# Kernel tuning notes

Measured on AMD Instinct MI355X. Metric: run time of the kernel, lower is better.

## Reference

```python
import jax
jax.config.update("jax_enable_x64", True)
import jax.numpy as jnp
import numpy as np

CKA_WEIGHT = 0.1


def _group_cka_sum(feats):
    """feats: [F, N, D] float. Returns sum of pairwise CKA over all (i,j) pairs.

    Faithful to CKASR: K = X X^T with zeroed diagonal, unbiased HSIC
    (Song et al. estimator), CKA[i,j] = HSIC(Ki,Kj)/sqrt(HSIC(Ki,Ki)HSIC(Kj,Kj)).
    All pairwise loops are batched into einsums.
    """
    F, N, D = feats.shape
    X = feats.reshape(F, N, D).astype(jnp.float64)
    K = jnp.einsum('fnd,fmd->fnm', X, X)                 # [F,N,N] Gram
    K = K * (1.0 - jnp.eye(N, dtype=K.dtype))            # fill_diagonal_(0)
    # HSIC(Ki, Kj) = 1/(N(N-3)) * ( tr(Ki Kj)
    #   + sum(Ki) sum(Kj) / ((N-1)(N-2))
    #   - 2/(N-2) * <rowsum(Ki), rowsum(Kj)> )
    trKL = jnp.einsum('iab,jab->ij', K, K)               # tr(Ki Kj), K symmetric
    s = jnp.sum(K, axis=(1, 2))                          # [F] total sums
    r = jnp.sum(K, axis=2)                               # [F,N] row sums
    rr = jnp.einsum('ia,ja->ij', r, r)                   # [F,F]
    hsic = (trKL + jnp.outer(s, s) / ((N - 1) * (N - 2))
            - 2.0 * rr / (N - 2)) / (N * (N - 3))        # [F,F]
    d = jnp.sqrt(jnp.diagonal(hsic))                     # [F]
    cka = hsic / (d[:, None] * d[None, :])
    return jnp.sum(cka)


def setup_inputs() -> dict:
    key = jax.random.key(0)
    k1, k2, k3, k4 = jax.random.split(key, 4)
    N, C = 64, 1000
    output = jax.random.normal(k1, (N, C), dtype=jnp.float32)
    target = jax.random.randint(k2, (N,), 0, C, dtype=jnp.int64)
    feats_a = jax.random.normal(k3, (3, N, 65536), dtype=jnp.float32)
    feats_b = jax.random.normal(k4, (4, N, 32768), dtype=jnp.float32)
    return {"output": output, "target": target,
            "feats_a": feats_a, "feats_b": feats_b}


def reference(output, target, feats_a, feats_b):
    N = output.shape[0]
    logp = jax.nn.log_softmax(output.astype(jnp.float32), axis=-1)
    ce = -jnp.mean(logp[jnp.arange(N), target])           # CrossEntropyLoss (mean)
    cka = _group_cka_sum(feats_a) + _group_cka_sum(feats_b)
    loss = ce + CKA_WEIGHT * cka.astype(jnp.float32)
    return (loss, output)
```

## Files before the change

### kernel.cpp

```cpp
#include <hip/hip_runtime.h>
#include <hip/hip_bf16.h>
#include <math.h>

typedef __attribute__((ext_vector_type(8))) short short8;
typedef __attribute__((ext_vector_type(4))) float f32x4;

#define PSTRIDE 4160
#define SLAB_A_F 8388608u
#define SLAB_B_F 4194304u

__device__ __forceinline__ unsigned int bf16_rn(float x) {
    unsigned int u = __float_as_uint(x);
    return (u + 0x7FFFu + ((u >> 16) & 1u)) >> 16;
}

__global__ __launch_bounds__(256) void ce_kernel(
    const float* __restrict__ logits, const int* __restrict__ target,
    float* __restrict__ out_copy, float* __restrict__ ce_rows)
{
    const int row = blockIdx.x;
    const float* x = logits + row * 1000;
    const int t = threadIdx.x;
    __shared__ float red[256];

    float m = -INFINITY;
    for (int i = t; i < 1000; i += 256) {
        float v = x[i];
        out_copy[row * 1000 + i] = v;
        m = fmaxf(m, v);
    }
    red[t] = m; __syncthreads();
    for (int s = 128; s > 0; s >>= 1) {
        if (t < s) red[t] = fmaxf(red[t], red[t + s]);
        __syncthreads();
    }
    m = red[0];
    __syncthreads();

    float ssum = 0.f;
    for (int i = t; i < 1000; i += 256) ssum += expf(x[i] - m);
    red[t] = ssum; __syncthreads();
    for (int s = 128; s > 0; s >>= 1) {
        if (t < s) red[t] += red[t + s];
        __syncthreads();
    }
    if (t == 0) {
        double lse = (double)m + log((double)red[0]);
        int tg = target[row];
        ce_rows[row] = (float)(-((double)x[tg] - lse));
    }
}

__global__ __launch_bounds__(256) void repack_kernel(
    const float* __restrict__ A, const float* __restrict__ B,
    char* __restrict__ slab, int nfA, int nfB)
{
    const int uA = nfA * 512;
    const int uTot = uA + nfB * 256;
    const int t = threadIdx.x;

    for (int u = blockIdx.x; u < uTot; u += gridDim.x) {
        const float* xr;
        char* slabF;
        int row, seg, D;
        if (u < uA) {
            int f = u >> 9, rem = u & 511;
            seg = rem & 7; row = rem >> 3; D = 65536;
            xr = A + ((size_t)(f * 64 + row)) * D;
            slabF = slab + (size_t)f * SLAB_A_F;
        } else {
            int v = u - uA;
            int f = v >> 8, rem = v & 255;
            seg = rem & 3; row = rem >> 2; D = 32768;
            xr = B + ((size_t)(f * 64 + row)) * D;
            slabF = slab + (size_t)nfA * SLAB_A_F + (size_t)f * SLAB_B_F;
        }
        const int k0 = seg * 8192;
        float4 va[4], vb[4];
#pragma unroll
        for (int i = 0; i < 4; ++i) {
            const float* p = xr + k0 + i * 2048 + t * 8;
            va[i] = *(const float4*)p;
            vb[i] = *(const float4*)(p + 4);
        }
#pragma unroll
        for (int i = 0; i < 4; ++i) {
            float vv[8] = {va[i].x, va[i].y, va[i].z, va[i].w,
                           vb[i].x, vb[i].y, vb[i].z, vb[i].w};
            short8 hv;
#pragma unroll
            for (int j = 0; j < 8; ++j) hv[j] = (short)bf16_rn(vv[j]);
            int kg = k0 + i * 2048 + t * 8;
            int chunk = kg >> 9, kk = kg & 511;
            *(short8*)(slabF + (size_t)chunk * 65536 + row * 1024 + kk * 2) = hv;
        }
    }
}

__global__ __launch_bounds__(256) void gram_kernel(
    const char* __restrict__ slab, float* __restrict__ partials,
    int nfA, int nfB)
{
    __shared__ float kbuf[4096];
    const int blk = blockIdx.x;
    const int f = blk >> 6, local = blk & 63;

    const char* slabF;
    int c0, nchunk;
    if (f < nfA) {
        slabF = slab + (size_t)f * SLAB_A_F;
        c0 = local * 2; nchunk = 2;
    } else {
        slabF = slab + (size_t)nfA * SLAB_A_F + (size_t)(f - nfA) * SLAB_B_F;
        c0 = local; nchunk = 1;
    }

    const int t = threadIdx.x;
    const int wave = t >> 6, lane = t & 63;
    const int m = lane & 15, quad = lane >> 4;
    const int loff = wave * 256 + quad * 16;

    f32x4 acc[4][4];
#pragma unroll
    for (int i = 0; i < 4; ++i)
#pragma unroll
        for (int j = 0; j < 4; ++j) acc[i][j] = (f32x4)0.f;

    for (int ci = 0; ci < nchunk; ++ci) {
        const char* cb = slabF + (size_t)(c0 + ci) * 65536;
        short8 fr[4][4];
#pragma unroll
        for (int s = 0; s < 4; ++s)
#pragma unroll
            for (int tm = 0; tm < 4; ++tm)
                fr[s][tm] = *(const short8*)(cb + (tm * 16 + m) * 1024
                                             + loff + s * 64);
#pragma unroll
        for (int s = 0; s < 4; ++s)
#pragma unroll
            for (int tm = 0; tm < 4; ++tm)
#pragma unroll
                for (int tn = 0; tn < 4; ++tn)
                    acc[tm][tn] = __builtin_amdgcn_mfma_f32_16x16x32_bf16(
                        fr[s][tm], fr[s][tn], acc[tm][tn], 0, 0, 0);
    }

    __syncthreads();
    if (wave == 0) {
#pragma unroll
        for (int tm = 0; tm < 4; ++tm)
#pragma unroll
            for (int tn = 0; tn < 4; ++tn)
#pragma unroll
                for (int r = 0; r < 4; ++r)
                    kbuf[(tm * 16 + quad * 4 + r) * 64 + tn * 16 + m] = acc[tm][tn][r];
    }
    __syncthreads();
    if (wave != 0) {
#pragma unroll
        for (int tm = 0; tm < 4; ++tm)
#pragma unroll
            for (int tn = 0; tn < 4; ++tn)
#pragma unroll
                for (int r = 0; r < 4; ++r)
                    atomicAdd(&kbuf[(tm * 16 + quad * 4 + r) * 64 + tn * 16 + m],
                              acc[tm][tn][r]);
    }
    __syncthreads();

    float4* outp = (float4*)(partials + (size_t)blk * PSTRIDE);
    const float4* kb4 = (const float4*)kbuf;
    for (int e = t; e < 1024; e += 256) outp[e] = kb4[e];
}

__global__ __launch_bounds__(256) void reduce_kernel(
    const float* __restrict__ partials, float* __restrict__ K, int singleF)
{
    __shared__ double red[256];
    int f, eblk, base;
    if (singleF < 0) { f = blockIdx.x >> 6; eblk = blockIdx.x & 63; base = f * 64; }
    else             { f = singleF; eblk = blockIdx.x; base = 0; }
    const int e = (eblk << 6) + (threadIdx.x & 63);
    const int jg = threadIdx.x >> 6;

    double s0 = 0.0, s1 = 0.0;
    for (int j = jg; j < 64; j += 8) {
        s0 += (double)partials[(size_t)(base + j) * PSTRIDE + e];
        s1 += (double)partials[(size_t)(base + j + 4) * PSTRIDE + e];
    }
    red[threadIdx.x] = s0 + s1;
    __syncthreads();
    if (jg == 0) {
        double tot = red[threadIdx.x] + red[threadIdx.x + 64]
                   + red[threadIdx.x + 128] + red[threadIdx.x + 192];
        int rr = e >> 6, cc = e & 63;
        K[f * 4096 + e] = (rr == cc) ? 0.f : (float)tot;
    }
}

__global__ __launch_bounds__(256) void hsic_kernel(
    const float* __restrict__ K, double* __restrict__ hsic_out)
{
    const int p = blockIdx.x;
    int i, j;
    if (p < 9) { i = p / 3; j = p % 3; }
    else       { int q = p - 9; i = 3 + q / 4; j = 3 + q % 4; }
    const float* Ki = K + i * 4096;
    const float* Kj = K + j * 4096;
    const int t = threadIdx.x;

    __shared__ double red[256];
    __shared__ double ri[64], rj[64];

    double local = 0.0;
    for (int e = t; e < 4096; e += 256)
        local += (double)Ki[e] * (double)Kj[e];
    red[t] = local; __syncthreads();
    for (int s = 128; s > 0; s >>= 1) {
        if (t < s) red[t] += red[t + s];
        __syncthreads();
    }

    if (t < 64) {
        double s = 0.0;
        for (int mc = 0; mc < 64; ++mc) s += (double)Ki[t * 64 + mc];
        ri[t] = s;
    } else if (t < 128) {
        int n = t - 64;
        double s = 0.0;
        for (int mc = 0; mc < 64; ++mc) s += (double)Kj[n * 64 + mc];
        rj[n] = s;
    }
    __syncthreads();

    if (t == 0) {
        double tr = red[0];
        double rr = 0.0, si = 0.0, sj = 0.0;
        for (int n = 0; n < 64; ++n) {
            rr += ri[n] * rj[n];
            si += ri[n];
            sj += rj[n];
        }
        const double N = 64.0;
        const double c1 = (N - 1.0) * (N - 2.0);
        const double c2 = N - 2.0;
        const double c3 = N * (N - 3.0);
        hsic_out[p] = (tr + si * sj / c1 - 2.0 * rr / c2) / c3;
    }
}

__global__ __launch_bounds__(64) void final_kernel(
    const double* __restrict__ hsic, const float* __restrict__ ce_rows,
    float* __restrict__ out_loss)
{
    if (threadIdx.x != 0) return;
    double ce = 0.0;
    for (int n = 0; n < 64; ++n) ce += (double)ce_rows[n];
    ce /= 64.0;

    double cka_total = 0.0;
    for (int i = 0; i < 3; ++i)
        for (int j = 0; j < 3; ++j)
            cka_total += hsic[i * 3 + j] / sqrt(hsic[i * 3 + i] * hsic[j * 3 + j]);
    for (int i = 0; i < 4; ++i)
        for (int j = 0; j < 4; ++j)
            cka_total += hsic[9 + i * 4 + j] / sqrt(hsic[9 + i * 4 + i] * hsic[9 + j * 4 + j]);

    out_loss[0] = (float)(ce + 0.1 * cka_total);
}

extern "C" void kernel_launch(void* const* d_in, const int* in_sizes, int n_in,
                              void* d_out, int out_size, void* d_ws, size_t ws_size,
                              hipStream_t stream)
{
    const float* output  = (const float*)d_in[0];
    const int*   target  = (const int*)d_in[1];
    const float* feats_a = (const float*)d_in[2];
    const float* feats_b = (const float*)d_in[3];
    float* out = (float*)d_out;

    char* ws = (char*)d_ws;
    float*  K       = (float*)ws;
    float*  ce_rows = (float*)(ws + 114688);
    double* hsic    = (double*)(ws + 114944);
    char*   slab    = ws + 131072;

    const size_t slabAll = 3 * (size_t)SLAB_A_F + 4 * (size_t)SLAB_B_F;
    const size_t partMain = (size_t)448 * PSTRIDE * 4;
    const size_t mainNeed = 131072 + slabAll + partMain;

    hipLaunchKernelGGL(ce_kernel, dim3(64), dim3(256), 0, stream,
                       output, target, out + 1, ce_rows);

    if (ws_size >= mainNeed) {
        float* partials = (float*)(slab + slabAll);
        hipLaunchKernelGGL(repack_kernel, dim3(1280), dim3(256), 0, stream,
                           feats_a, feats_b, slab, 3, 4);
        hipLaunchKernelGGL(gram_kernel, dim3(448), dim3(256), 0, stream,
                           (const char*)slab, partials, 3, 4);
        hipLaunchKernelGGL(reduce_kernel, dim3(448), dim3(256), 0, stream,
                           partials, K, -1);
    } else {
        float* partials = (float*)(slab + SLAB_A_F);
        for (int f = 0; f < 7; ++f) {
            if (f < 3) {
                const float* X = feats_a + (size_t)f * 64 * 65536;
                hipLaunchKernelGGL(repack_kernel, dim3(256), dim3(256), 0, stream,
                                   X, (const float*)nullptr, slab, 1, 0);
                hipLaunchKernelGGL(gram_kernel, dim3(64), dim3(256), 0, stream,
                                   (const char*)slab, partials, 1, 0);
            } else {
                const float* X = feats_b + (size_t)(f - 3) * 64 * 32768;
                hipLaunchKernelGGL(repack_kernel, dim3(128), dim3(256), 0, stream,
                                   (const float*)nullptr, X, slab, 0, 1);
                hipLaunchKernelGGL(gram_kernel, dim3(64), dim3(256), 0, stream,
                                   (const char*)slab, partials, 0, 1);
            }
            hipLaunchKernelGGL(reduce_kernel, dim3(64), dim3(256), 0, stream,
                               partials, K, f);
        }
    }

    hipLaunchKernelGGL(hsic_kernel, dim3(25), dim3(256), 0, stream, K, hsic);
    hipLaunchKernelGGL(final_kernel, dim3(1), dim3(64), 0, stream,
                       hsic, ce_rows, out);
}
```

Measured before the change: 177.9 us.

## Repack features into MFMA-fragment-ready layout via LDS and prefetch in gram

The repack kernel now stages a 64-row by 256-column tile in shared memory and writes bf16 data in the exact per-lane fragment order the gram kernel consumes. Gram loads become fully contiguous 16-byte-per-lane reads, and the next chunk is loaded while the current chunk's MFMAs run. The hsic and final kernels are merged into a single one-block kernel that computes row sums once and uses wave shuffles, which removes a launch and redundant row-sum work. The cost is an LDS round trip in repack and a serial 25-pair loop in one block for the final stage.

```diff
diff --git a/kernel.cpp b/kernel.cpp
--- a/kernel.cpp
+++ b/kernel.cpp
@@ -6,8 +6,10 @@
 typedef __attribute__((ext_vector_type(4))) float f32x4;
 
 #define PSTRIDE 4160
+#define CHUNK_B 16384
 #define SLAB_A_F 8388608u
 #define SLAB_B_F 4194304u
+#define LROW 528
 
 __device__ __forceinline__ unsigned int bf16_rn(float x) {
     unsigned int u = __float_as_uint(x);
@@ -55,44 +57,51 @@
     const float* __restrict__ A, const float* __restrict__ B,
     char* __restrict__ slab, int nfA, int nfB)
 {
-    const int uA = nfA * 512;
-    const int uTot = uA + nfB * 256;
-    const int t = threadIdx.x;
-
-    for (int u = blockIdx.x; u < uTot; u += gridDim.x) {
-        const float* xr;
-        char* slabF;
-        int row, seg, D;
-        if (u < uA) {
-            int f = u >> 9, rem = u & 511;
-            seg = rem & 7; row = rem >> 3; D = 65536;
-            xr = A + ((size_t)(f * 64 + row)) * D;
-            slabF = slab + (size_t)f * SLAB_A_F;
-        } else {
-            int v = u - uA;
-            int f = v >> 8, rem = v & 255;
-            seg = rem & 3; row = rem >> 2; D = 32768;
-            xr = B + ((size_t)(f * 64 + row)) * D;
-            slabF = slab + (size_t)nfA * SLAB_A_F + (size_t)f * SLAB_B_F;
-        }
-        const int k0 = seg * 8192;
-        float4 va[4], vb[4];
-#pragma unroll
-        for (int i = 0; i < 4; ++i) {
-            const float* p = xr + k0 + i * 2048 + t * 8;
-            va[i] = *(const float4*)p;
-            vb[i] = *(const float4*)(p + 4);
-        }
-#pragma unroll
-        for (int i = 0; i < 4; ++i) {
-            float vv[8] = {va[i].x, va[i].y, va[i].z, va[i].w,
-                           vb[i].x, vb[i].y, vb[i].z, vb[i].w};
-            short8 hv;
-#pragma unroll
-            for (int j = 0; j < 8; ++j) hv[j] = (short)bf16_rn(vv[j]);
-            int kg = k0 + i * 2048 + t * 8;
-            int chunk = kg >> 9, kk = kg & 511;
-            *(short8*)(slabF + (size_t)chunk * 65536 + row * 1024 + kk * 2) = hv;
+    __shared__ __align__(16) char lds[64 * LROW];
+
+    const int uA = nfA * 256;
+    const int u = blockIdx.x;
+    const float* xbase; char* slabF; int D, span;
+    if (u < uA) {
+        int f = u >> 8; span = u & 255; D = 65536;
+        xbase = A + (size_t)f * 64 * D;
+        slabF = slab + (size_t)f * SLAB_A_F;
+    } else {
+        int v = u - uA;
+        int f = v >> 7; span = v & 127; D = 32768;
+        xbase = B + (size_t)f * 64 * D;
+        slabF = slab + (size_t)nfA * SLAB_A_F + (size_t)f * SLAB_B_F;
+    }
+    const int k0 = span * 256;
+    const int wave = threadIdx.x >> 6, lane = threadIdx.x & 63;
+
+    float4 v[16];
+#pragma unroll
+    for (int i = 0; i < 16; ++i) {
+        int row = wave * 16 + i;
+        v[i] = *(const float4*)(xbase + (size_t)row * D + k0 + lane * 4);
+    }
+#pragma unroll
+    for (int i = 0; i < 16; ++i) {
+        int row = wave * 16 + i;
+        uint2 h;
+        h.x = bf16_rn(v[i].x) | (bf16_rn(v[i].y) << 16);
+        h.y = bf16_rn(v[i].z) | (bf16_rn(v[i].w) << 16);
+        *(uint2*)(lds + row * LROW + lane * 8) = h;
+    }
+    __syncthreads();
+
+    const int m = lane & 15;
+#pragma unroll
+    for (int cc = 0; cc < 2; ++cc) {
+        const int c = span * 2 + cc;
+#pragma unroll
+        for (int tm = 0; tm < 4; ++tm) {
+            int row = tm * 16 + m;
+            int kl = cc * 128 + wave * 32 + ((lane >> 4) << 3);
+            short8 s = *(const short8*)(lds + row * LROW + kl * 2);
+            *(short8*)(slabF + (size_t)c * CHUNK_B + wave * 4096
+                       + tm * 1024 + lane * 16) = s;
         }
     }
 }
@@ -105,20 +114,18 @@
     const int blk = blockIdx.x;
     const int f = blk >> 6, local = blk & 63;
 
-    const char* slabF;
-    int c0, nchunk;
+    const char* slabF; int c0, nchunk;
     if (f < nfA) {
-        slabF = slab + (size_t)f * SLAB_A_F;
-        c0 = local * 2; nchunk = 2;
+        slabF = slab + (size_t)f * SLAB_A_F; c0 = local * 8; nchunk = 8;
     } else {
         slabF = slab + (size_t)nfA * SLAB_A_F + (size_t)(f - nfA) * SLAB_B_F;
-        c0 = local; nchunk = 1;
+        c0 = local * 4; nchunk = 4;
     }
 
     const int t = threadIdx.x;
     const int wave = t >> 6, lane = t & 63;
     const int m = lane & 15, quad = lane >> 4;
-    const int loff = wave * 256 + quad * 16;
+    const char* base = slabF + (size_t)c0 * CHUNK_B + wave * 4096 + lane * 16;
 
     f32x4 acc[4][4];
 #pragma unroll
@@ -126,23 +133,26 @@
 #pragma unroll
         for (int j = 0; j < 4; ++j) acc[i][j] = (f32x4)0.f;
 
+    short8 cur[4], nxt[4];
+#pragma unroll
+    for (int tm = 0; tm < 4; ++tm)
+        cur[tm] = *(const short8*)(base + tm * 1024);
+
     for (int ci = 0; ci < nchunk; ++ci) {
-        const char* cb = slabF + (size_t)(c0 + ci) * 65536;
-        short8 fr[4][4];
-#pragma unroll
-        for (int s = 0; s < 4; ++s)
+        if (ci + 1 < nchunk) {
+            const char* nb = base + (size_t)(ci + 1) * CHUNK_B;
 #pragma unroll
             for (int tm = 0; tm < 4; ++tm)
-                fr[s][tm] = *(const short8*)(cb + (tm * 16 + m) * 1024
-                                             + loff + s * 64);
-#pragma unroll
-        for (int s = 0; s < 4; ++s)
-#pragma unroll
-            for (int tm = 0; tm < 4; ++tm)
-#pragma unroll
-                for (int tn = 0; tn < 4; ++tn)
-                    acc[tm][tn] = __builtin_amdgcn_mfma_f32_16x16x32_bf16(
-                        fr[s][tm], fr[s][tn], acc[tm][tn], 0, 0, 0);
+                nxt[tm] = *(const short8*)(nb + tm * 1024);
+        }
+#pragma unroll
+        for (int tm = 0; tm < 4; ++tm)
+#pragma unroll
+            for (int tn = 0; tn < 4; ++tn)
+                acc[tm][tn] = __builtin_amdgcn_mfma_f32_16x16x32_bf16(
+                    cur[tm], cur[tn], acc[tm][tn], 0, 0, 0);
+#pragma unroll
+        for (int tm = 0; tm < 4; ++tm) cur[tm] = nxt[tm];
     }
 
     __syncthreads();
@@ -198,75 +208,82 @@
     }
 }
 
-__global__ __launch_bounds__(256) void hsic_kernel(
-    const float* __restrict__ K, double* __restrict__ hsic_out)
-{
-    const int p = blockIdx.x;
-    int i, j;
-    if (p < 9) { i = p / 3; j = p % 3; }
-    else       { int q = p - 9; i = 3 + q / 4; j = 3 + q % 4; }
-    const float* Ki = K + i * 4096;
-    const float* Kj = K + j * 4096;
+__global__ __launch_bounds__(256) void hsic_final_kernel(
+    const float* __restrict__ K, const float* __restrict__ ce_rows,
+    float* __restrict__ out_loss)
+{
+    __shared__ double rsum[7][64];
+    __shared__ double ssum[7];
+    __shared__ double trKL[25];
+    __shared__ double wred[4];
     const int t = threadIdx.x;
 
-    __shared__ double red[256];
-    __shared__ double ri[64], rj[64];
-
-    double local = 0.0;
-    for (int e = t; e < 4096; e += 256)
-        local += (double)Ki[e] * (double)Kj[e];
-    red[t] = local; __syncthreads();
-    for (int s = 128; s > 0; s >>= 1) {
-        if (t < s) red[t] += red[t + s];
+    for (int task = t; task < 448; task += 256) {
+        int f = task >> 6, n = task & 63;
+        const float* Kf = K + f * 4096 + n * 64;
+        double s = 0.0;
+        for (int mc = 0; mc < 64; ++mc) s += (double)Kf[mc];
+        rsum[f][n] = s;
+    }
+    __syncthreads();
+    if (t < 7) {
+        double s = 0.0;
+        for (int n = 0; n < 64; ++n) s += rsum[t][n];
+        ssum[t] = s;
+    }
+
+    for (int p = 0; p < 25; ++p) {
+        int i, j;
+        if (p < 9) { i = p / 3; j = p % 3; }
+        else       { int q = p - 9; i = 3 + q / 4; j = 3 + q % 4; }
+        const float* Ki = K + i * 4096;
+        const float* Kj = K + j * 4096;
+        double local = 0.0;
+        for (int e = t; e < 4096; e += 256)
+            local += (double)Ki[e] * (double)Kj[e];
+        for (int off = 32; off > 0; off >>= 1)
+            local += __shfl_down(local, off);
+        if ((t & 63) == 0) wred[t >> 6] = local;
         __syncthreads();
-    }
-
-    if (t < 64) {
-        double s = 0.0;
-        for (int mc = 0; mc < 64; ++mc) s += (double)Ki[t * 64 + mc];
-        ri[t] = s;
-    } else if (t < 128) {
-        int n = t - 64;
-        double s = 0.0;
-        for (int mc = 0; mc < 64; ++mc) s += (double)Kj[n * 64 + mc];
-        rj[n] = s;
-    }
-    __syncthreads();
+        if (t == 0) trKL[p] = wred[0] + wred[1] + wred[2] + wred[3];
+        __syncthreads();
+    }
 
     if (t == 0) {
-        double tr = red[0];
-        double rr = 0.0, si = 0.0, sj = 0.0;
-        for (int n = 0; n < 64; ++n) {
-            rr += ri[n] * rj[n];
-            si += ri[n];
-            sj += rj[n];
-        }
+        double ce = 0.0;
+        for (int n = 0; n < 64; ++n) ce += (double)ce_rows[n];
+        ce /= 64.0;
+
         const double N = 64.0;
         const double c1 = (N - 1.0) * (N - 2.0);
         const double c2 = N - 2.0;
         const double c3 = N * (N - 3.0);
-        hsic_out[p] = (tr + si * sj / c1 - 2.0 * rr / c2) / c3;
-    }
-}
-
-__global__ __launch_bounds__(64) void final_kernel(
-    const double* __restrict__ hsic, const float* __restrict__ ce_rows,
-    float* __restrict__ out_loss)
-{
-    if (threadIdx.x != 0) return;
-    double ce = 0.0;
-    for (int n = 0; n < 64; ++n) ce += (double)ce_rows[n];
-    ce /= 64.0;
-
-    double cka_total = 0.0;
-    for (int i = 0; i < 3; ++i)
-        for (int j = 0; j < 3; ++j)
-            cka_total += hsic[i * 3 + j] / sqrt(hsic[i * 3 + i] * hsic[j * 3 + j]);
-    for (int i = 0; i < 4; ++i)
-        for (int j = 0; j < 4; ++j)
-            cka_total += hsic[9 + i * 4 + j] / sqrt(hsic[9 + i * 4 + i] * hsic[9 + j * 4 + j]);
-
-    out_loss[0] = (float)(ce + 0.1 * cka_total);
+        double cka_total = 0.0;
+
+        double hA[3][3];
+        for (int p = 0; p < 9; ++p) {
+            int i = p / 3, j = p % 3;
+            double rr = 0.0;
+            for (int n = 0; n < 64; ++n) rr += rsum[i][n] * rsum[j][n];
+            hA[i][j] = (trKL[p] + ssum[i] * ssum[j] / c1 - 2.0 * rr / c2) / c3;
+        }
+        for (int i = 0; i < 3; ++i)
+            for (int j = 0; j < 3; ++j)
+                cka_total += hA[i][j] / sqrt(hA[i][i] * hA[j][j]);
+
+        double hB[4][4];
+        for (int q = 0; q < 16; ++q) {
+            int i = q / 4, j = q % 4;
+            double rr = 0.0;
+            for (int n = 0; n < 64; ++n) rr += rsum[3 + i][n] * rsum[3 + j][n];
+            hB[i][j] = (trKL[9 + q] + ssum[3 + i] * ssum[3 + j] / c1 - 2.0 * rr / c2) / c3;
+        }
+        for (int i = 0; i < 4; ++i)
+            for (int j = 0; j < 4; ++j)
+                cka_total += hB[i][j] / sqrt(hB[i][i] * hB[j][j]);
+
+        out_loss[0] = (float)(ce + 0.1 * cka_total);
+    }
 }
 
 extern "C" void kernel_launch(void* const* d_in, const int* in_sizes, int n_in,
@@ -282,7 +299,6 @@
     char* ws = (char*)d_ws;
     float*  K       = (float*)ws;
     float*  ce_rows = (float*)(ws + 114688);
-    double* hsic    = (double*)(ws + 114944);
     char*   slab    = ws + 131072;
 
     const size_t slabAll = 3 * (size_t)SLAB_A_F + 4 * (size_t)SLAB_B_F;
@@ -321,7 +337,6 @@
         }
     }
 
-    hipLaunchKernelGGL(hsic_kernel, dim3(25), dim3(256), 0, stream, K, hsic);
-    hipLaunchKernelGGL(final_kernel, dim3(1), dim3(64), 0, stream,
-                       hsic, ce_rows, out);
-}
+    hipLaunchKernelGGL(hsic_final_kernel, dim3(1), dim3(256), 0, stream,
+                       K, ce_rows, out);
+}
```

After: 246.4 us. +38.5%, slower.
